# Performance work log

Measured on AMD Instinct MI355X. Metric: run time of the kernel, lower is better.

Reference implementation:

```python
import jax, jax.numpy as jnp
import numpy as np

N_NODES = 20000
OUT_DEG = 16
E = N_NODES * OUT_DEG          # 320000 directed edges
F = 20                          # edge_features
H3 = 3 * F


def _lin(key, fan_in, fan_out):
    kw, kb = jax.random.split(key)
    bound = 1.0 / np.sqrt(fan_in)
    W = jax.random.uniform(kw, (fan_in, fan_out), jnp.float32, -bound, bound)
    b = jax.random.uniform(kb, (fan_out,), jnp.float32, -bound, bound)
    return W, b


def setup_inputs() -> dict:
    key = jax.random.key(0)
    rng = np.random.default_rng(0)
    # graph: every node has exactly OUT_DEG out-edges, no self-loops
    src = np.repeat(np.arange(N_NODES, dtype=np.int64), OUT_DEG)
    dst = (src + 1 + rng.integers(0, N_NODES - 1, size=E)) % N_NODES
    edge_index = jnp.asarray(np.stack([src, dst]), dtype=jnp.int32)
    # edge adjacency per _build_edge_adj: edge i=(u->v) pairs with each out-edge j of v.
    # Edges are grouped by src, so out-edges of node v are [v*OUT_DEG, v*OUT_DEG+OUT_DEG).
    # No self-loops => i != j always, so exactly E*OUT_DEG pairs.
    adj_src = jnp.asarray(np.repeat(np.arange(E, dtype=np.int64), OUT_DEG).astype(np.int32))
    adj_nbr = jnp.asarray((dst[:, None] * OUT_DEG + np.arange(OUT_DEG)).reshape(-1).astype(np.int32))

    ks = jax.random.split(key, 8)
    edge_attr = jax.random.normal(ks[0], (E, F), jnp.float32)
    msg_W1, msg_b1 = _lin(ks[1], 2 * F, 32)
    msg_W2, msg_b2 = _lin(ks[2], 32, F)
    # torch GRUCell params: weight_ih/hh are [3H, H]
    bound = 1.0 / np.sqrt(F)
    g = jax.random.split(ks[3], 4)
    gru_Wih = jax.random.uniform(g[0], (H3, F), jnp.float32, -bound, bound)
    gru_Whh = jax.random.uniform(g[1], (H3, F), jnp.float32, -bound, bound)
    gru_bih = jax.random.uniform(g[2], (H3,), jnp.float32, -bound, bound)
    gru_bhh = jax.random.uniform(g[3], (H3,), jnp.float32, -bound, bound)
    ro_W1, ro_b1 = _lin(ks[4], F, 64)
    ro_W2, ro_b2 = _lin(ks[5], 64, 32)
    ro_W3, ro_b3 = _lin(ks[6], 32, 1)
    return {
        'edge_attr': edge_attr,
        'msg_W1': msg_W1, 'msg_b1': msg_b1, 'msg_W2': msg_W2, 'msg_b2': msg_b2,
        'gru_Wih': gru_Wih, 'gru_Whh': gru_Whh, 'gru_bih': gru_bih, 'gru_bhh': gru_bhh,
        'ro_W1': ro_W1, 'ro_b1': ro_b1, 'ro_W2': ro_W2, 'ro_b2': ro_b2,
        'ro_W3': ro_W3, 'ro_b3': ro_b3,
        'edge_index': edge_index, 'adj_src': adj_src, 'adj_nbr': adj_nbr,
    }


def reference(edge_attr, msg_W1, msg_b1, msg_W2, msg_b2,
              gru_Wih, gru_Whh, gru_bih, gru_bhh,
              ro_W1, ro_b1, ro_W2, ro_b2, ro_W3, ro_b3,
              edge_index, adj_src, adj_nbr):
    num_e = edge_attr.shape[0]

    def step(h, _):
        h_i = h[adj_src]                       # [P, F] gather
        h_j = h[adj_nbr]                       # [P, F] gather
        m = jnp.concatenate([h_i, h_j], axis=-1)  # [P, 2F]
        m = jax.nn.selu(m @ msg_W1 + msg_b1) @ msg_W2 + msg_b2  # [P, F]
        agg = jax.ops.segment_sum(m, adj_src, num_segments=num_e)  # scatter_add
        # torch.nn.GRUCell(agg, h)
        gi = agg @ gru_Wih.T + gru_bih
        gh = h @ gru_Whh.T + gru_bhh
        i_r, i_z, i_n = jnp.split(gi, 3, axis=-1)
        h_r, h_z, h_n = jnp.split(gh, 3, axis=-1)
        r = jax.nn.sigmoid(i_r + h_r)
        z = jax.nn.sigmoid(i_z + h_z)
        n = jnp.tanh(i_n + r * h_n)
        return (1.0 - z) * n + z * h, None

    h_t, _ = jax.lax.scan(step, edge_attr, None, length=4)
    h_base = h_t[:num_e]  # num_edges == E here
    x = jax.nn.selu(h_base @ ro_W1 + ro_b1)
    x = jax.nn.selu(x @ ro_W2 + ro_b2)
    w = jax.nn.softplus(x @ ro_W3 + ro_b3).squeeze(-1) + 0.1
    return jnp.clip(w, 0.1, 10.0)
```

## Files before the change

### kernel.cpp

```cpp
#include <hip/hip_runtime.h>
#include <hip/hip_fp16.h>

#define E_EDGES 320000
#define NF 20

typedef float v4 __attribute__((ext_vector_type(4)));
typedef float v2f __attribute__((ext_vector_type(2)));

#if defined(__has_builtin)
# if __has_builtin(__builtin_elementwise_fma)
#  define EWFMA(a,b,c) __builtin_elementwise_fma((a),(b),(c))
# endif
#endif
#ifndef EWFMA
# define EWFMA(a,b,c) ((a)*(b)+(c))
#endif
#if defined(__has_builtin)
# if __has_builtin(__builtin_elementwise_max)
#  define EWMAX(a,b) __builtin_elementwise_max((a),(b))
#  define EWMIN(a,b) __builtin_elementwise_min((a),(b))
# endif
#endif

#if defined(__has_builtin)
# if __has_builtin(__builtin_amdgcn_exp2f)
#  define EX2F(x) __builtin_amdgcn_exp2f(x)
# endif
#endif
#ifndef EX2F
# define EX2F(x) exp2f(x)
#endif

#define LOG2E_F 1.4426950408889634f
#define SELU_SCALE 1.0507009873554805f
#define SELU_ALPHA 1.6732632423543772f
#define SELU_KA (SELU_SCALE * SELU_ALPHA)
#define SELU_SC2 (SELU_SCALE / LOG2E_F)

__device__ __forceinline__ v4 bc4(float s) { return (v4){s, s, s, s}; }
__device__ __forceinline__ v4 v4z() { return (v4){0.f, 0.f, 0.f, 0.f}; }

__device__ __forceinline__ float selu_f(float x) {
    const float scale = SELU_SCALE;
    const float alpha = SELU_ALPHA;
    float p = fmaxf(x, 0.f);
    float m = fminf(x, 0.f);
    float e = __expf(m);
    return fmaf(scale, p, scale * alpha * (e - 1.f));
}
__device__ __forceinline__ float sigmoid_f(float x) {
    return 1.f / (1.f + __expf(-x));
}
__device__ __forceinline__ v4 selu4(v4 x) {
    const float scale = SELU_SCALE;
    const float ka = SELU_KA;
#ifdef EWMAX
    v4 p = EWMAX(x, v4z());
    v4 m = EWMIN(x, v4z());
#else
    v4 p = {fmaxf(x.x,0.f), fmaxf(x.y,0.f), fmaxf(x.z,0.f), fmaxf(x.w,0.f)};
    v4 m = {fminf(x.x,0.f), fminf(x.y,0.f), fminf(x.z,0.f), fminf(x.w,0.f)};
#endif
    v4 e = {__expf(m.x), __expf(m.y), __expf(m.z), __expf(m.w)};
    return EWFMA(bc4(scale), p, EWFMA(bc4(ka), e, bc4(-ka)));
}

__device__ __forceinline__ float hsum4(v4 x) {
    v2f lo = __builtin_shufflevector(x, x, 0, 1);
    v2f hi = __builtin_shufflevector(x, x, 2, 3);
    v2f h = lo + hi;
    return h.x + h.y;
}

__device__ __forceinline__ float dot20v(v4 a0, v4 a1, v4 a2, v4 a3, v4 a4,
                                        const v4* __restrict__ w) {
    v4 w0 = w[0], w1 = w[1], w2 = w[2], w3 = w[3], w4 = w[4];
    v4 x = a0 * w0;
    x = EWFMA(a1, w1, x); x = EWFMA(a2, w2, x);
    x = EWFMA(a3, w3, x); x = EWFMA(a4, w4, x);
    return hsum4(x);
}
__device__ __forceinline__ void dot20_dualv(const v4* __restrict__ w,
    v4 a0, v4 a1, v4 a2, v4 a3, v4 a4,
    v4 b0, v4 b1, v4 b2, v4 b3, v4 b4,
    float& r0, float& r1)
{
    v4 w0 = w[0], w1 = w[1], w2 = w[2], w3 = w[3], w4 = w[4];
    v4 xa = a0 * w0;
    xa = EWFMA(a1, w1, xa); xa = EWFMA(a2, w2, xa);
    xa = EWFMA(a3, w3, xa); xa = EWFMA(a4, w4, xa);
    v4 xb = b0 * w0;
    xb = EWFMA(b1, w1, xb); xb = EWFMA(b2, w2, xb);
    xb = EWFMA(b3, w3, xb); xb = EWFMA(b4, w4, xb);
    r0 = hsum4(xa);
    r1 = hsum4(xb);
}
__device__ __forceinline__ void h8_to_v4x2(uint4 r, v4& lo, v4& hi) {
    float2 fa = __half22float2(__builtin_bit_cast(__half2, r.x));
    float2 fb = __half22float2(__builtin_bit_cast(__half2, r.y));
    float2 fc = __half22float2(__builtin_bit_cast(__half2, r.z));
    float2 fd = __half22float2(__builtin_bit_cast(__half2, r.w));
    lo = (v4){fa.x, fa.y, fb.x, fb.y};
    hi = (v4){fc.x, fc.y, fd.x, fd.y};
}
__device__ __forceinline__ uint4 f8_to_h8(v4 lo, v4 hi) {
    uint4 r;
    r.x = __builtin_bit_cast(unsigned, __floats2half2_rn(lo.x, lo.y));
    r.y = __builtin_bit_cast(unsigned, __floats2half2_rn(lo.z, lo.w));
    r.z = __builtin_bit_cast(unsigned, __floats2half2_rn(hi.x, hi.y));
    r.w = __builtin_bit_cast(unsigned, __floats2half2_rn(hi.z, hi.w));
    return r;
}

#define FOR20(X) \
  X(0, v0.x) X(1, v0.y) X(2, v0.z) X(3, v0.w) \
  X(4, v1.x) X(5, v1.y) X(6, v1.z) X(7, v1.w) \
  X(8, v2.x) X(9, v2.y) X(10, v2.z) X(11, v2.w) \
  X(12, v3.x) X(13, v3.y) X(14, v3.z) X(15, v3.w) \
  X(16, v4v.x) X(17, v4v.y) X(18, v4v.z) X(19, v4v.w)

#define FOR20_2(X) \
  X(0, va0.x, vb0.x) X(1, va0.y, vb0.y) X(2, va0.z, vb0.z) X(3, va0.w, vb0.w) \
  X(4, va1.x, vb1.x) X(5, va1.y, vb1.y) X(6, va1.z, vb1.z) X(7, va1.w, vb1.w) \
  X(8, va2.x, vb2.x) X(9, va2.y, vb2.y) X(10, va2.z, vb2.z) X(11, va2.w, vb2.w) \
  X(12, va3.x, vb3.x) X(13, va3.y, vb3.y) X(14, va3.z, vb3.z) X(15, va3.w, vb3.w) \
  X(16, va4.x, vb4.x) X(17, va4.y, vb4.y) X(18, va4.z, vb4.z) X(19, va4.w, vb4.w)

#define FOR8S2(X) \
  X(0, sa0.x, sb0.x) X(1, sa0.y, sb0.y) X(2, sa0.z, sb0.z) X(3, sa0.w, sb0.w) \
  X(4, sa1.x, sb1.x) X(5, sa1.y, sb1.y) X(6, sa1.z, sb1.z) X(7, sa1.w, sb1.w)

__global__ void __launch_bounds__(256) kernel_B0(
    const float* __restrict__ h, const float* __restrict__ W1,
    const float* __restrict__ b1, __half* __restrict__ B)
{
    __shared__ __align__(16) float sw[640];
    __shared__ __align__(16) float sbias[32];
    for (int i = threadIdx.x; i < 640; i += 256) sw[i] = W1[640 + i] * LOG2E_F;
    if (threadIdx.x < 32) sbias[threadIdx.x] = b1[threadIdx.x] * LOG2E_F;
    __syncthreads();
    int e = blockIdx.x * 256 + threadIdx.x;
    const v4* hp = reinterpret_cast<const v4*>(h + (size_t)e * NF);
    v4 v0 = hp[0], v1 = hp[1], v2 = hp[2], v3 = hp[3], v4v = hp[4];
    const v4* bi = reinterpret_cast<const v4*>(sbias);
    v4 c0 = bi[0], c1 = bi[1], c2 = bi[2], c3 = bi[3],
       c4 = bi[4], c5 = bi[5], c6 = bi[6], c7 = bi[7];
    #define BSTEP(f, hf) { v4 t_ = bc4(hf); const v4* w_ = (const v4*)&sw[(f)*32]; \
        c0 = EWFMA(t_, w_[0], c0); c1 = EWFMA(t_, w_[1], c1); \
        c2 = EWFMA(t_, w_[2], c2); c3 = EWFMA(t_, w_[3], c3); \
        c4 = EWFMA(t_, w_[4], c4); c5 = EWFMA(t_, w_[5], c5); \
        c6 = EWFMA(t_, w_[6], c6); c7 = EWFMA(t_, w_[7], c7); }
    FOR20(BSTEP)
    #undef BSTEP
    uint4* Bp = reinterpret_cast<uint4*>(B + (size_t)e * 32);
    Bp[0] = f8_to_h8(c0, c1); Bp[1] = f8_to_h8(c2, c3);
    Bp[2] = f8_to_h8(c4, c5); Bp[3] = f8_to_h8(c6, c7);
}

template<bool WRITEB>
__global__ void __launch_bounds__(256) kernel_stepT(
    const float* __restrict__ h_in, float* __restrict__ h_out,
    const __half* __restrict__ Br, const int* __restrict__ dst,
    const float* __restrict__ W1, const float* __restrict__ b1,
    const float* __restrict__ W2, const float* __restrict__ b2,
    const float* __restrict__ Wih, const float* __restrict__ Whh,
    const float* __restrict__ bih, const float* __restrict__ bhh,
    __half* __restrict__ Bw)
{
    __shared__ __align__(16) float sW1[640];
    __shared__ __align__(16) float sW1h[640];
    __shared__ __align__(16) float sb1h[32];
    __shared__ __align__(16) float sW2[640];
    __shared__ __align__(16) float sb2v[20];
    __shared__ __align__(16) float sCorr[20];
    __shared__ __align__(16) float sWih[1200];
    __shared__ __align__(16) float sWhh[1200];
    __shared__ float sbih[60];
    __shared__ float sbhh[60];
    for (int i = threadIdx.x; i < 640; i += 256) {
        sW1[i] = W1[i] * LOG2E_F;
        sW2[i] = W2[i];
        if (WRITEB) sW1h[i] = W1[640 + i] * LOG2E_F;
    }
    for (int i = threadIdx.x; i < 1200; i += 256) { sWih[i] = Wih[i]; sWhh[i] = Whh[i]; }
    if (threadIdx.x < 20) sb2v[threadIdx.x] = b2[threadIdx.x];
    else if (threadIdx.x >= 64 && threadIdx.x < 124) sbih[threadIdx.x - 64] = bih[threadIdx.x - 64];
    else if (threadIdx.x >= 128 && threadIdx.x < 188) sbhh[threadIdx.x - 128] = bhh[threadIdx.x - 128];
    else if (WRITEB && threadIdx.x >= 192 && threadIdx.x < 224)
        sb1h[threadIdx.x - 192] = b1[threadIdx.x - 192] * LOG2E_F;
    __syncthreads();
    if (threadIdx.x < 20) {
        float s = 0.f;
        #pragma unroll
        for (int o = 0; o < 32; o++) s += sW2[o * 20 + threadIdx.x];
        sCorr[threadIdx.x] = 16.f * (sb2v[threadIdx.x] - SELU_KA * s);
    }
    __syncthreads();

    int t = blockIdx.x * 256 + threadIdx.x;
    int p = t >> 2;
    int q = t & 3;
    int ob = q * 8;
    int e0 = p * 2, e1 = p * 2 + 1;

    int2 dd = *reinterpret_cast<const int2*>(dst + e0);
    int d0 = dd.x, d1 = dd.y;

    const v4* hp0 = reinterpret_cast<const v4*>(h_in + (size_t)e0 * NF);
    const v4* hp1 = reinterpret_cast<const v4*>(h_in + (size_t)e1 * NF);
    v4 va0 = hp0[0], va1 = hp0[1], va2 = hp0[2], va3 = hp0[3], va4 = hp0[4];
    v4 vb0 = hp1[0], vb1 = hp1[1], vb2 = hp1[2], vb3 = hp1[3], vb4 = hp1[4];

    v4 aa0 = v4z(), aa1 = v4z(), ab0 = v4z(), ab1 = v4z();
    #define ASTEP2(f, h0, h1) { const v4* w_ = (const v4*)&sW1[(f)*32 + ob]; \
        v4 w0_ = w_[0], w1_ = w_[1]; \
        v4 t0_ = bc4(h0), t1_ = bc4(h1); \
        aa0 = EWFMA(t0_, w0_, aa0); aa1 = EWFMA(t0_, w1_, aa1); \
        ab0 = EWFMA(t1_, w0_, ab0); ab1 = EWFMA(t1_, w1_, ab1); }
    FOR20_2(ASTEP2)
    #undef ASTEP2

    const uint4* Bp0 = reinterpret_cast<const uint4*>(Br) + (size_t)d0 * 64 + q;
    const uint4* Bp1 = reinterpret_cast<const uint4*>(Br) + (size_t)d1 * 64 + q;
    v4 sa0 = v4z(), sa1 = v4z(), sb0 = v4z(), sb1 = v4z();
    {
        v4 kav = bc4(SELU_KA), scv = bc4(SELU_SC2), z4 = v4z();
        #define SELUACC(s_, a_, b_) { v4 x_ = (a_) + (b_); \
            v4 p_ = EWMAX(x_, z4); v4 m_ = EWMIN(x_, z4); \
            v4 e_ = {EX2F(m_.x), EX2F(m_.y), EX2F(m_.z), EX2F(m_.w)}; \
            s_ = EWFMA(kav, e_, s_); s_ = EWFMA(scv, p_, s_); }
        #pragma unroll 4
        for (int k = 0; k < 16; k++) {
            uint4 rA = Bp0[k * 4];
            uint4 rB = Bp1[k * 4];
            v4 loA, hiA, loB, hiB;
            h8_to_v4x2(rA, loA, hiA);
            h8_to_v4x2(rB, loB, hiB);
            SELUACC(sa0, aa0, loA);
            SELUACC(sa1, aa1, hiA);
            SELUACC(sb0, ab0, loB);
            SELUACC(sb1, ab1, hiB);
        }
        #undef SELUACC
    }

    v4 ga0 = v4z(), ga1 = v4z(), ga2 = v4z(), ga3 = v4z(), ga4 = v4z();
    v4 gb0 = v4z(), gb1 = v4z(), gb2 = v4z(), gb3 = v4z(), gb4 = v4z();
    #define AGGS2(j, c0_, c1_) { const v4* w_ = (const v4*)&sW2[(ob + (j)) * 20]; \
        v4 w0_ = w_[0], w1_ = w_[1], w2_ = w_[2], w3_ = w_[3], w4_ = w_[4]; \
        v4 u_ = bc4(c0_), vv_ = bc4(c1_); \
        ga0 = EWFMA(u_, w0_, ga0); ga1 = EWFMA(u_, w1_, ga1); ga2 = EWFMA(u_, w2_, ga2); \
        ga3 = EWFMA(u_, w3_, ga3); ga4 = EWFMA(u_, w4_, ga4); \
        gb0 = EWFMA(vv_, w0_, gb0); gb1 = EWFMA(vv_, w1_, gb1); gb2 = EWFMA(vv_, w2_, gb2); \
        gb3 = EWFMA(vv_, w3_, gb3); gb4 = EWFMA(vv_, w4_, gb4); }
    FOR8S2(AGGS2)
    #undef AGGS2

    #define BF1(r_, m_) { v4 t_ = { __shfl_xor(r_.x, m_), __shfl_xor(r_.y, m_), \
                                    __shfl_xor(r_.z, m_), __shfl_xor(r_.w, m_) }; \
                          r_ = r_ + t_; }
    #define BFLY(m_) BF1(ga0, m_) BF1(ga1, m_) BF1(ga2, m_) BF1(ga3, m_) BF1(ga4, m_) \
                     BF1(gb0, m_) BF1(gb1, m_) BF1(gb2, m_) BF1(gb3, m_) BF1(gb4, m_)
    BFLY(1)
    BFLY(2)
    #undef BFLY
    #undef BF1

    {
        const v4* cp = reinterpret_cast<const v4*>(sCorr);
        v4 c0 = cp[0], c1 = cp[1], c2 = cp[2], c3 = cp[3], c4 = cp[4];
        ga0 = ga0 + c0; ga1 = ga1 + c1; ga2 = ga2 + c2; ga3 = ga3 + c3; ga4 = ga4 + c4;
        gb0 = gb0 + c0; gb1 = gb1 + c1; gb2 = gb2 + c2; gb3 = gb3 + c3; gb4 = gb4 + c4;
    }

    v4 ba0, ba1, bb0, bb1;
    if (WRITEB) {
        const v4* b1p = reinterpret_cast<const v4*>(&sb1h[ob]);
        ba0 = b1p[0]; ba1 = b1p[1];
        bb0 = b1p[0]; bb1 = b1p[1];
    }

    for (int i = 0; i < 5; i++) {
        int c = q * 5 + i;
        float ir0, ir1, iz0, iz1, in0, in1, hr0, hr1, hz0, hz1, hn0, hn1;
        dot20_dualv((const v4*)&sWih[c * 20],        ga0, ga1, ga2, ga3, ga4,
                    gb0, gb1, gb2, gb3, gb4, ir0, ir1);
        dot20_dualv((const v4*)&sWih[(20 + c) * 20], ga0, ga1, ga2, ga3, ga4,
                    gb0, gb1, gb2, gb3, gb4, iz0, iz1);
        dot20_dualv((const v4*)&sWih[(40 + c) * 20], ga0, ga1, ga2, ga3, ga4,
                    gb0, gb1, gb2, gb3, gb4, in0, in1);
        dot20_dualv((const v4*)&sWhh[c * 20],        va0, va1, va2, va3, va4,
                    vb0, vb1, vb2, vb3, vb4, hr0, hr1);
        dot20_dualv((const v4*)&sWhh[(20 + c) * 20], va0, va1, va2, va3, va4,
                    vb0, vb1, vb2, vb3, vb4, hz0, hz1);
        dot20_dualv((const v4*)&sWhh[(40 + c) * 20], va0, va1, va2, va3, va4,
                    vb0, vb1, vb2, vb3, vb4, hn0, hn1);
        float bi_r = sbih[c], bi_z = sbih[20 + c], bi_n = sbih[40 + c];
        float bh_r = sbhh[c], bh_z = sbhh[20 + c], bh_n = sbhh[40 + c];
        float nh0, nh1;
        {
            float r = sigmoid_f(bi_r + ir0 + bh_r + hr0);
            float z = sigmoid_f(bi_z + iz0 + bh_z + hz0);
            float xn = bi_n + in0 + r * (bh_n + hn0);
            xn = fminf(fmaxf(xn, -20.f), 20.f);
            float tt = __expf(2.f * xn);
            float n = (tt - 1.f) / (tt + 1.f);
            float hc = h_in[(size_t)e0 * NF + c];
            nh0 = (1.f - z) * n + z * hc;
            h_out[(size_t)e0 * NF + c] = nh0;
        }
        {
            float r = sigmoid_f(bi_r + ir1 + bh_r + hr1);
            float z = sigmoid_f(bi_z + iz1 + bh_z + hz1);
            float xn = bi_n + in1 + r * (bh_n + hn1);
            xn = fminf(fmaxf(xn, -20.f), 20.f);
            float tt = __expf(2.f * xn);
            float n = (tt - 1.f) / (tt + 1.f);
            float hc = h_in[(size_t)e1 * NF + c];
            nh1 = (1.f - z) * n + z * hc;
            h_out[(size_t)e1 * NF + c] = nh1;
        }
        if (WRITEB) {
            #pragma unroll
            for (int qq = 0; qq < 4; ++qq) {
                float f0 = __shfl(nh0, qq, 4);
                float f1 = __shfl(nh1, qq, 4);
                const v4* wp = reinterpret_cast<const v4*>(&sW1h[(qq * 5 + i) * 32 + ob]);
                v4 w0 = wp[0], w1 = wp[1];
                v4 t0 = bc4(f0), t1 = bc4(f1);
                ba0 = EWFMA(t0, w0, ba0); ba1 = EWFMA(t0, w1, ba1);
                bb0 = EWFMA(t1, w0, bb0); bb1 = EWFMA(t1, w1, bb1);
            }
        }
    }
    if (WRITEB) {
        uint4* Bo = reinterpret_cast<uint4*>(Bw);
        Bo[(size_t)e0 * 4 + q] = f8_to_h8(ba0, ba1);
        Bo[(size_t)e1 * 4 + q] = f8_to_h8(bb0, bb1);
    }
}

__global__ void __launch_bounds__(256) kernel_readout(
    const float* __restrict__ h,
    const float* __restrict__ W1, const float* __restrict__ b1,
    const float* __restrict__ W2, const float* __restrict__ b2,
    const float* __restrict__ W3, const float* __restrict__ b3,
    float* __restrict__ out)
{
    __shared__ __align__(16) float sW1t[1280];
    __shared__ float sb1[64];
    __shared__ __align__(16) float sW2[2048];
    __shared__ __align__(16) float sb2v[32];
    __shared__ __align__(16) float sW3[32];
    __shared__ float sb3;
    for (int i = threadIdx.x; i < 1280; i += 256) {
        int f = i >> 6, o = i & 63;
        sW1t[o * 20 + f] = W1[i];
    }
    for (int i = threadIdx.x; i < 2048; i += 256) sW2[i] = W2[i];
    if (threadIdx.x < 64) sb1[threadIdx.x] = b1[threadIdx.x];
    else if (threadIdx.x >= 64 && threadIdx.x < 96) sb2v[threadIdx.x - 64] = b2[threadIdx.x - 64];
    else if (threadIdx.x >= 96 && threadIdx.x < 128) sW3[threadIdx.x - 96] = W3[threadIdx.x - 96];
    if (threadIdx.x == 128) sb3 = b3[0];
    __syncthreads();

    int e = blockIdx.x * 256 + threadIdx.x;
    const v4* hp = reinterpret_cast<const v4*>(h + (size_t)e * NF);
    v4 v0 = hp[0], v1 = hp[1], v2 = hp[2], v3 = hp[3], v4v = hp[4];

    const v4* b2p = reinterpret_cast<const v4*>(sb2v);
    v4 x20 = b2p[0], x21 = b2p[1], x22 = b2p[2], x23 = b2p[3],
       x24 = b2p[4], x25 = b2p[5], x26 = b2p[6], x27 = b2p[7];
    for (int o = 0; o < 64; o++) {
        float x1 = sb1[o] + dot20v(v0, v1, v2, v3, v4v, (const v4*)&sW1t[o * 20]);
        x1 = selu_f(x1);
        v4 xb = bc4(x1);
        const v4* w = (const v4*)&sW2[o * 32];
        x20 = EWFMA(xb, w[0], x20); x21 = EWFMA(xb, w[1], x21);
        x22 = EWFMA(xb, w[2], x22); x23 = EWFMA(xb, w[3], x23);
        x24 = EWFMA(xb, w[4], x24); x25 = EWFMA(xb, w[5], x25);
        x26 = EWFMA(xb, w[6], x26); x27 = EWFMA(xb, w[7], x27);
    }
    const v4* w3p = reinterpret_cast<const v4*>(sW3);
    v4 accv = selu4(x20) * w3p[0];
    accv = EWFMA(selu4(x21), w3p[1], accv);
    accv = EWFMA(selu4(x22), w3p[2], accv);
    accv = EWFMA(selu4(x23), w3p[3], accv);
    accv = EWFMA(selu4(x24), w3p[4], accv);
    accv = EWFMA(selu4(x25), w3p[5], accv);
    accv = EWFMA(selu4(x26), w3p[6], accv);
    accv = EWFMA(selu4(x27), w3p[7], accv);
    float acc = sb3 + hsum4(accv);
    float sp = fmaxf(acc, 0.f) + log1pf(__expf(-fabsf(acc)));
    float w = sp + 0.1f;
    w = fminf(fmaxf(w, 0.1f), 10.f);
    out[e] = w;
}

extern "C" void kernel_launch(void* const* d_in, const int* in_sizes, int n_in,
                              void* d_out, int out_size, void* d_ws, size_t ws_size,
                              hipStream_t stream) {
    const float* edge_attr = (const float*)d_in[0];
    const float* msg_W1   = (const float*)d_in[1];
    const float* msg_b1   = (const float*)d_in[2];
    const float* msg_W2   = (const float*)d_in[3];
    const float* msg_b2   = (const float*)d_in[4];
    const float* gru_Wih  = (const float*)d_in[5];
    const float* gru_Whh  = (const float*)d_in[6];
    const float* gru_bih  = (const float*)d_in[7];
    const float* gru_bhh  = (const float*)d_in[8];
    const float* ro_W1    = (const float*)d_in[9];
    const float* ro_b1    = (const float*)d_in[10];
    const float* ro_W2    = (const float*)d_in[11];
    const float* ro_b2    = (const float*)d_in[12];
    const float* ro_W3    = (const float*)d_in[13];
    const float* ro_b3    = (const float*)d_in[14];
    const int* edge_index = (const int*)d_in[15];
    const int* dst = edge_index + E_EDGES;

    float*  h_ws = (float*)d_ws;
    __half* BtA  = (__half*)(h_ws + (size_t)E_EDGES * NF);
    __half* BtB  = BtA + (size_t)E_EDGES * 32;

    size_t need = (size_t)E_EDGES * NF * sizeof(float)
                + 2 * (size_t)E_EDGES * 32 * sizeof(__half);
    bool fused = ws_size >= need;

    dim3 block(256);
    dim3 gridB(E_EDGES / 256);
    dim3 gridS(E_EDGES * 2 / 256);

    kernel_B0<<<gridB, block, 0, stream>>>(edge_attr, msg_W1, msg_b1, BtA);

    const float* hin = edge_attr;
    __half* Bin = BtA;
    __half* Bout = BtB;
    for (int s = 0; s < 4; s++) {
        if (!fused && s > 0)
            kernel_B0<<<gridB, block, 0, stream>>>(hin, msg_W1, msg_b1, BtA);
        if (fused && s < 3) {
            kernel_stepT<true><<<gridS, block, 0, stream>>>(hin, h_ws, Bin, dst,
                msg_W1, msg_b1, msg_W2, msg_b2, gru_Wih, gru_Whh, gru_bih, gru_bhh,
                Bout);
            __half* tmp = Bin; Bin = Bout; Bout = tmp;
        } else {
            kernel_stepT<false><<<gridS, block, 0, stream>>>(hin, h_ws, Bin, dst,
                msg_W1, msg_b1, msg_W2, msg_b2, gru_Wih, gru_Whh, gru_bih, gru_bhh,
                nullptr);
        }
        hin = h_ws;
    }
    kernel_readout<<<gridB, block, 0, stream>>>(h_ws, ro_W1, ro_b1, ro_W2, ro_b2,
                                                ro_W3, ro_b3, (float*)d_out);
}
```

Before: 554.8 us.

## Fuse final GRU step with readout MLP and use DPP lane reductions

The last message-passing step is merged with the readout MLP in one kernel. Each block keeps its updated hidden states in shared memory, reloads the readout weights into the same shared buffer, and splits the readout across two threads per edge. This removes one launch and the write and re-read of the final h through global memory. Cross-lane shuffles in the butterfly reduction and the broadcast are replaced with DPP moves, at the cost of added synchronisation and register pressure in the fused kernel.

```diff
diff --git a/kernel.cpp b/kernel.cpp
--- a/kernel.cpp
+++ b/kernel.cpp
@@ -40,6 +40,21 @@
 __device__ __forceinline__ v4 bc4(float s) { return (v4){s, s, s, s}; }
 __device__ __forceinline__ v4 v4z() { return (v4){0.f, 0.f, 0.f, 0.f}; }
 
+#define DPP_XOR1 0xB1
+#define DPP_XOR2 0x4E
+template<int CTRL>
+__device__ __forceinline__ float dppf(float x) {
+    return __builtin_bit_cast(float,
+        __builtin_amdgcn_update_dpp(0, __builtin_bit_cast(int, x), CTRL, 0xF, 0xF, true));
+}
+template<int CTRL>
+__device__ __forceinline__ v4 dpp4(v4 x) {
+    v4 r;
+    r.x = dppf<CTRL>(x.x); r.y = dppf<CTRL>(x.y);
+    r.z = dppf<CTRL>(x.z); r.w = dppf<CTRL>(x.w);
+    return r;
+}
+
 __device__ __forceinline__ float selu_f(float x) {
     const float scale = SELU_SCALE;
     const float alpha = SELU_ALPHA;
@@ -72,14 +87,6 @@
     return h.x + h.y;
 }
 
-__device__ __forceinline__ float dot20v(v4 a0, v4 a1, v4 a2, v4 a3, v4 a4,
-                                        const v4* __restrict__ w) {
-    v4 w0 = w[0], w1 = w[1], w2 = w[2], w3 = w[3], w4 = w[4];
-    v4 x = a0 * w0;
-    x = EWFMA(a1, w1, x); x = EWFMA(a2, w2, x);
-    x = EWFMA(a3, w3, x); x = EWFMA(a4, w4, x);
-    return hsum4(x);
-}
 __device__ __forceinline__ void dot20_dualv(const v4* __restrict__ w,
     v4 a0, v4 a1, v4 a2, v4 a3, v4 a4,
     v4 b0, v4 b1, v4 b2, v4 b3, v4 b4,
@@ -256,15 +263,16 @@
     FOR8S2(AGGS2)
     #undef AGGS2
 
-    #define BF1(r_, m_) { v4 t_ = { __shfl_xor(r_.x, m_), __shfl_xor(r_.y, m_), \
-                                    __shfl_xor(r_.z, m_), __shfl_xor(r_.w, m_) }; \
-                          r_ = r_ + t_; }
-    #define BFLY(m_) BF1(ga0, m_) BF1(ga1, m_) BF1(ga2, m_) BF1(ga3, m_) BF1(ga4, m_) \
-                     BF1(gb0, m_) BF1(gb1, m_) BF1(gb2, m_) BF1(gb3, m_) BF1(gb4, m_)
-    BFLY(1)
-    BFLY(2)
+    #define BFLY(CTRL) { \
+        ga0 = ga0 + dpp4<CTRL>(ga0); ga1 = ga1 + dpp4<CTRL>(ga1); \
+        ga2 = ga2 + dpp4<CTRL>(ga2); ga3 = ga3 + dpp4<CTRL>(ga3); \
+        ga4 = ga4 + dpp4<CTRL>(ga4); \
+        gb0 = gb0 + dpp4<CTRL>(gb0); gb1 = gb1 + dpp4<CTRL>(gb1); \
+        gb2 = gb2 + dpp4<CTRL>(gb2); gb3 = gb3 + dpp4<CTRL>(gb3); \
+        gb4 = gb4 + dpp4<CTRL>(gb4); }
+    BFLY(DPP_XOR1)
+    BFLY(DPP_XOR2)
     #undef BFLY
-    #undef BF1
 
     {
         const v4* cp = reinterpret_cast<const v4*>(sCorr);
@@ -321,16 +329,16 @@
             h_out[(size_t)e1 * NF + c] = nh1;
         }
         if (WRITEB) {
-            #pragma unroll
-            for (int qq = 0; qq < 4; ++qq) {
-                float f0 = __shfl(nh0, qq, 4);
-                float f1 = __shfl(nh1, qq, 4);
-                const v4* wp = reinterpret_cast<const v4*>(&sW1h[(qq * 5 + i) * 32 + ob]);
-                v4 w0 = wp[0], w1 = wp[1];
-                v4 t0 = bc4(f0), t1 = bc4(f1);
-                ba0 = EWFMA(t0, w0, ba0); ba1 = EWFMA(t0, w1, ba1);
-                bb0 = EWFMA(t1, w0, bb0); bb1 = EWFMA(t1, w1, bb1);
-            }
+            #define WB1(qq) { \
+                float f0_ = dppf<(qq)*0x55>(nh0); \
+                float f1_ = dppf<(qq)*0x55>(nh1); \
+                const v4* wp_ = reinterpret_cast<const v4*>(&sW1h[((qq)*5 + i) * 32 + ob]); \
+                v4 w0_ = wp_[0], w1_ = wp_[1]; \
+                v4 t0_ = bc4(f0_), t1_ = bc4(f1_); \
+                ba0 = EWFMA(t0_, w0_, ba0); ba1 = EWFMA(t0_, w1_, ba1); \
+                bb0 = EWFMA(t1_, w0_, bb0); bb1 = EWFMA(t1_, w1_, bb1); }
+            WB1(0) WB1(1) WB1(2) WB1(3)
+            #undef WB1
         }
     }
     if (WRITEB) {
@@ -340,61 +348,237 @@
     }
 }
 
-__global__ void __launch_bounds__(256) kernel_readout(
-    const float* __restrict__ h,
-    const float* __restrict__ W1, const float* __restrict__ b1,
-    const float* __restrict__ W2, const float* __restrict__ b2,
-    const float* __restrict__ W3, const float* __restrict__ b3,
+__global__ void __launch_bounds__(256) kernel_step_ro(
+    const float* __restrict__ h_in,
+    const __half* __restrict__ Br, const int* __restrict__ dst,
+    const float* __restrict__ W1, const float* __restrict__ W2, const float* __restrict__ b2,
+    const float* __restrict__ Wih, const float* __restrict__ Whh,
+    const float* __restrict__ bih, const float* __restrict__ bhh,
+    const float* __restrict__ roW1, const float* __restrict__ rob1,
+    const float* __restrict__ roW2, const float* __restrict__ rob2,
+    const float* __restrict__ roW3, const float* __restrict__ rob3,
     float* __restrict__ out)
 {
-    __shared__ __align__(16) float sW1t[1280];
-    __shared__ float sb1[64];
-    __shared__ __align__(16) float sW2[2048];
-    __shared__ __align__(16) float sb2v[32];
-    __shared__ __align__(16) float sW3[32];
-    __shared__ float sb3;
-    for (int i = threadIdx.x; i < 1280; i += 256) {
-        int f = i >> 6, o = i & 63;
-        sW1t[o * 20 + f] = W1[i];
-    }
-    for (int i = threadIdx.x; i < 2048; i += 256) sW2[i] = W2[i];
-    if (threadIdx.x < 64) sb1[threadIdx.x] = b1[threadIdx.x];
-    else if (threadIdx.x >= 64 && threadIdx.x < 96) sb2v[threadIdx.x - 64] = b2[threadIdx.x - 64];
-    else if (threadIdx.x >= 96 && threadIdx.x < 128) sW3[threadIdx.x - 96] = W3[threadIdx.x - 96];
-    if (threadIdx.x == 128) sb3 = b3[0];
+    __shared__ __align__(16) float S[3840];
+    __shared__ __align__(16) float sh[2560];
+    float* sW1  = S;
+    float* sW2  = S + 640;
+    float* sb2v = S + 1280;
+    float* sCorr= S + 1300;
+    float* sWih = S + 1320;
+    float* sWhh = S + 2520;
+    float* sbih = S + 3720;
+    float* sbhh = S + 3780;
+
+    for (int i = threadIdx.x; i < 640; i += 256) {
+        sW1[i] = W1[i] * LOG2E_F;
+        sW2[i] = W2[i];
+    }
+    for (int i = threadIdx.x; i < 1200; i += 256) { sWih[i] = Wih[i]; sWhh[i] = Whh[i]; }
+    if (threadIdx.x < 20) sb2v[threadIdx.x] = b2[threadIdx.x];
+    else if (threadIdx.x >= 64 && threadIdx.x < 124) sbih[threadIdx.x - 64] = bih[threadIdx.x - 64];
+    else if (threadIdx.x >= 128 && threadIdx.x < 188) sbhh[threadIdx.x - 128] = bhh[threadIdx.x - 128];
     __syncthreads();
-
-    int e = blockIdx.x * 256 + threadIdx.x;
-    const v4* hp = reinterpret_cast<const v4*>(h + (size_t)e * NF);
-    v4 v0 = hp[0], v1 = hp[1], v2 = hp[2], v3 = hp[3], v4v = hp[4];
-
-    const v4* b2p = reinterpret_cast<const v4*>(sb2v);
-    v4 x20 = b2p[0], x21 = b2p[1], x22 = b2p[2], x23 = b2p[3],
-       x24 = b2p[4], x25 = b2p[5], x26 = b2p[6], x27 = b2p[7];
-    for (int o = 0; o < 64; o++) {
-        float x1 = sb1[o] + dot20v(v0, v1, v2, v3, v4v, (const v4*)&sW1t[o * 20]);
-        x1 = selu_f(x1);
-        v4 xb = bc4(x1);
-        const v4* w = (const v4*)&sW2[o * 32];
-        x20 = EWFMA(xb, w[0], x20); x21 = EWFMA(xb, w[1], x21);
-        x22 = EWFMA(xb, w[2], x22); x23 = EWFMA(xb, w[3], x23);
-        x24 = EWFMA(xb, w[4], x24); x25 = EWFMA(xb, w[5], x25);
-        x26 = EWFMA(xb, w[6], x26); x27 = EWFMA(xb, w[7], x27);
-    }
-    const v4* w3p = reinterpret_cast<const v4*>(sW3);
-    v4 accv = selu4(x20) * w3p[0];
-    accv = EWFMA(selu4(x21), w3p[1], accv);
-    accv = EWFMA(selu4(x22), w3p[2], accv);
-    accv = EWFMA(selu4(x23), w3p[3], accv);
-    accv = EWFMA(selu4(x24), w3p[4], accv);
-    accv = EWFMA(selu4(x25), w3p[5], accv);
-    accv = EWFMA(selu4(x26), w3p[6], accv);
-    accv = EWFMA(selu4(x27), w3p[7], accv);
-    float acc = sb3 + hsum4(accv);
-    float sp = fmaxf(acc, 0.f) + log1pf(__expf(-fabsf(acc)));
-    float w = sp + 0.1f;
-    w = fminf(fmaxf(w, 0.1f), 10.f);
-    out[e] = w;
+    if (threadIdx.x < 20) {
+        float s = 0.f;
+        #pragma unroll
+        for (int o = 0; o < 32; o++) s += sW2[o * 20 + threadIdx.x];
+        sCorr[threadIdx.x] = 16.f * (sb2v[threadIdx.x] - SELU_KA * s);
+    }
+    __syncthreads();
+
+    int t = blockIdx.x * 256 + threadIdx.x;
+    int p = t >> 2;
+    int q = t & 3;
+    int ob = q * 8;
+    int e0 = p * 2, e1 = p * 2 + 1;
+    int lp = threadIdx.x >> 2;
+    int el0 = lp * 2, el1 = lp * 2 + 1;
+
+    int2 dd = *reinterpret_cast<const int2*>(dst + e0);
+    int d0 = dd.x, d1 = dd.y;
+
+    const v4* hp0 = reinterpret_cast<const v4*>(h_in + (size_t)e0 * NF);
+    const v4* hp1 = reinterpret_cast<const v4*>(h_in + (size_t)e1 * NF);
+    v4 va0 = hp0[0], va1 = hp0[1], va2 = hp0[2], va3 = hp0[3], va4 = hp0[4];
+    v4 vb0 = hp1[0], vb1 = hp1[1], vb2 = hp1[2], vb3 = hp1[3], vb4 = hp1[4];
+
+    v4 aa0 = v4z(), aa1 = v4z(), ab0 = v4z(), ab1 = v4z();
+    #define ASTEP2(f, h0, h1) { const v4* w_ = (const v4*)&sW1[(f)*32 + ob]; \
+        v4 w0_ = w_[0], w1_ = w_[1]; \
+        v4 t0_ = bc4(h0), t1_ = bc4(h1); \
+        aa0 = EWFMA(t0_, w0_, aa0); aa1 = EWFMA(t0_, w1_, aa1); \
+        ab0 = EWFMA(t1_, w0_, ab0); ab1 = EWFMA(t1_, w1_, ab1); }
+    FOR20_2(ASTEP2)
+    #undef ASTEP2
+
+    const uint4* Bp0 = reinterpret_cast<const uint4*>(Br) + (size_t)d0 * 64 + q;
+    const uint4* Bp1 = reinterpret_cast<const uint4*>(Br) + (size_t)d1 * 64 + q;
+    v4 sa0 = v4z(), sa1 = v4z(), sb0 = v4z(), sb1 = v4z();
+    {
+        v4 kav = bc4(SELU_KA), scv = bc4(SELU_SC2), z4 = v4z();
+        #define SELUACC(s_, a_, b_) { v4 x_ = (a_) + (b_); \
+            v4 p_ = EWMAX(x_, z4); v4 m_ = EWMIN(x_, z4); \
+            v4 e_ = {EX2F(m_.x), EX2F(m_.y), EX2F(m_.z), EX2F(m_.w)}; \
+            s_ = EWFMA(kav, e_, s_); s_ = EWFMA(scv, p_, s_); }
+        #pragma unroll 4
+        for (int k = 0; k < 16; k++) {
+            uint4 rA = Bp0[k * 4];
+            uint4 rB = Bp1[k * 4];
+            v4 loA, hiA, loB, hiB;
+            h8_to_v4x2(rA, loA, hiA);
+            h8_to_v4x2(rB, loB, hiB);
+            SELUACC(sa0, aa0, loA);
+            SELUACC(sa1, aa1, hiA);
+            SELUACC(sb0, ab0, loB);
+            SELUACC(sb1, ab1, hiB);
+        }
+        #undef SELUACC
+    }
+
+    v4 ga0 = v4z(), ga1 = v4z(), ga2 = v4z(), ga3 = v4z(), ga4 = v4z();
+    v4 gb0 = v4z(), gb1 = v4z(), gb2 = v4z(), gb3 = v4z(), gb4 = v4z();
+    #define AGGS2(j, c0_, c1_) { const v4* w_ = (const v4*)&sW2[(ob + (j)) * 20]; \
+        v4 w0_ = w_[0], w1_ = w_[1], w2_ = w_[2], w3_ = w_[3], w4_ = w_[4]; \
+        v4 u_ = bc4(c0_), vv_ = bc4(c1_); \
+        ga0 = EWFMA(u_, w0_, ga0); ga1 = EWFMA(u_, w1_, ga1); ga2 = EWFMA(u_, w2_, ga2); \
+        ga3 = EWFMA(u_, w3_, ga3); ga4 = EWFMA(u_, w4_, ga4); \
+        gb0 = EWFMA(vv_, w0_, gb0); gb1 = EWFMA(vv_, w1_, gb1); gb2 = EWFMA(vv_, w2_, gb2); \
+        gb3 = EWFMA(vv_, w3_, gb3); gb4 = EWFMA(vv_, w4_, gb4); }
+    FOR8S2(AGGS2)
+    #undef AGGS2
+
+    #define BFLY(CTRL) { \
+        ga0 = ga0 + dpp4<CTRL>(ga0); ga1 = ga1 + dpp4<CTRL>(ga1); \
+        ga2 = ga2 + dpp4<CTRL>(ga2); ga3 = ga3 + dpp4<CTRL>(ga3); \
+        ga4 = ga4 + dpp4<CTRL>(ga4); \
+        gb0 = gb0 + dpp4<CTRL>(gb0); gb1 = gb1 + dpp4<CTRL>(gb1); \
+        gb2 = gb2 + dpp4<CTRL>(gb2); gb3 = gb3 + dpp4<CTRL>(gb3); \
+        gb4 = gb4 + dpp4<CTRL>(gb4); }
+    BFLY(DPP_XOR1)
+    BFLY(DPP_XOR2)
+    #undef BFLY
+
+    {
+        const v4* cp = reinterpret_cast<const v4*>(sCorr);
+        v4 c0 = cp[0], c1 = cp[1], c2 = cp[2], c3 = cp[3], c4 = cp[4];
+        ga0 = ga0 + c0; ga1 = ga1 + c1; ga2 = ga2 + c2; ga3 = ga3 + c3; ga4 = ga4 + c4;
+        gb0 = gb0 + c0; gb1 = gb1 + c1; gb2 = gb2 + c2; gb3 = gb3 + c3; gb4 = gb4 + c4;
+    }
+
+    for (int i = 0; i < 5; i++) {
+        int c = q * 5 + i;
+        float ir0, ir1, iz0, iz1, in0, in1, hr0, hr1, hz0, hz1, hn0, hn1;
+        dot20_dualv((const v4*)&sWih[c * 20],        ga0, ga1, ga2, ga3, ga4,
+                    gb0, gb1, gb2, gb3, gb4, ir0, ir1);
+        dot20_dualv((const v4*)&sWih[(20 + c) * 20], ga0, ga1, ga2, ga3, ga4,
+                    gb0, gb1, gb2, gb3, gb4, iz0, iz1);
+        dot20_dualv((const v4*)&sWih[(40 + c) * 20], ga0, ga1, ga2, ga3, ga4,
+                    gb0, gb1, gb2, gb3, gb4, in0, in1);
+        dot20_dualv((const v4*)&sWhh[c * 20],        va0, va1, va2, va3, va4,
+                    vb0, vb1, vb2, vb3, vb4, hr0, hr1);
+        dot20_dualv((const v4*)&sWhh[(20 + c) * 20], va0, va1, va2, va3, va4,
+                    vb0, vb1, vb2, vb3, vb4, hz0, hz1);
+        dot20_dualv((const v4*)&sWhh[(40 + c) * 20], va0, va1, va2, va3, va4,
+                    vb0, vb1, vb2, vb3, vb4, hn0, hn1);
+        float bi_r = sbih[c], bi_z = sbih[20 + c], bi_n = sbih[40 + c];
+        float bh_r = sbhh[c], bh_z = sbhh[20 + c], bh_n = sbhh[40 + c];
+        {
+            float r = sigmoid_f(bi_r + ir0 + bh_r + hr0);
+            float z = sigmoid_f(bi_z + iz0 + bh_z + hz0);
+            float xn = bi_n + in0 + r * (bh_n + hn0);
+            xn = fminf(fmaxf(xn, -20.f), 20.f);
+            float tt = __expf(2.f * xn);
+            float n = (tt - 1.f) / (tt + 1.f);
+            float hc = h_in[(size_t)e0 * NF + c];
+            sh[el0 * 20 + c] = (1.f - z) * n + z * hc;
+        }
+        {
+            float r = sigmoid_f(bi_r + ir1 + bh_r + hr1);
+            float z = sigmoid_f(bi_z + iz1 + bh_z + hz1);
+            float xn = bi_n + in1 + r * (bh_n + hn1);
+            xn = fminf(fmaxf(xn, -20.f), 20.f);
+            float tt = __expf(2.f * xn);
+            float n = (tt - 1.f) / (tt + 1.f);
+            float hc = h_in[(size_t)e1 * NF + c];
+            sh[el1 * 20 + c] = (1.f - z) * n + z * hc;
+        }
+    }
+
+    __syncthreads();
+    for (int i = threadIdx.x; i < 1280; i += 256) S[i] = roW1[i];
+    for (int i = threadIdx.x; i < 2048; i += 256) S[1344 + i] = roW2[i];
+    {
+        int tx = threadIdx.x;
+        if (tx < 64) S[1280 + tx] = rob1[tx];
+        else if (tx < 96) S[3392 + (tx - 64)] = rob2[tx - 64];
+        else if (tx < 128) S[3424 + (tx - 96)] = roW3[tx - 96];
+        else if (tx == 128) S[3456] = rob3[0];
+    }
+    __syncthreads();
+
+    {
+        int el = threadIdx.x >> 1;
+        int half = threadIdx.x & 1;
+        int ob32 = half * 32;
+        const v4* hp = reinterpret_cast<const v4*>(&sh[el * 20]);
+        v4 v0 = hp[0], v1 = hp[1], v2 = hp[2], v3 = hp[3], v4v = hp[4];
+
+        const v4* b1p = reinterpret_cast<const v4*>(&S[1280 + ob32]);
+        v4 x0 = b1p[0], x1 = b1p[1], x2 = b1p[2], x3 = b1p[3],
+           x4 = b1p[4], x5 = b1p[5], x6 = b1p[6], x7 = b1p[7];
+        #define ROS(f, hf) { v4 t_ = bc4(hf); const v4* w_ = (const v4*)&S[(f)*64 + ob32]; \
+            x0 = EWFMA(t_, w_[0], x0); x1 = EWFMA(t_, w_[1], x1); \
+            x2 = EWFMA(t_, w_[2], x2); x3 = EWFMA(t_, w_[3], x3); \
+            x4 = EWFMA(t_, w_[4], x4); x5 = EWFMA(t_, w_[5], x5); \
+            x6 = EWFMA(t_, w_[6], x6); x7 = EWFMA(t_, w_[7], x7); }
+        FOR20(ROS)
+        #undef ROS
+        x0 = selu4(x0); x1 = selu4(x1); x2 = selu4(x2); x3 = selu4(x3);
+        x4 = selu4(x4); x5 = selu4(x5); x6 = selu4(x6); x7 = selu4(x7);
+
+        const v4* b2p = reinterpret_cast<const v4*>(&S[3392]);
+        v4 y0, y1, y2, y3, y4, y5, y6, y7;
+        if (half == 0) {
+            y0 = b2p[0]; y1 = b2p[1]; y2 = b2p[2]; y3 = b2p[3];
+            y4 = b2p[4]; y5 = b2p[5]; y6 = b2p[6]; y7 = b2p[7];
+        } else {
+            y0 = v4z(); y1 = v4z(); y2 = v4z(); y3 = v4z();
+            y4 = v4z(); y5 = v4z(); y6 = v4z(); y7 = v4z();
+        }
+        #define Y8(s_, o_) { const v4* w_ = reinterpret_cast<const v4*>(&S[1344 + (o_)*32]); \
+            v4 t_ = bc4(s_); \
+            y0 = EWFMA(t_, w_[0], y0); y1 = EWFMA(t_, w_[1], y1); \
+            y2 = EWFMA(t_, w_[2], y2); y3 = EWFMA(t_, w_[3], y3); \
+            y4 = EWFMA(t_, w_[4], y4); y5 = EWFMA(t_, w_[5], y5); \
+            y6 = EWFMA(t_, w_[6], y6); y7 = EWFMA(t_, w_[7], y7); }
+        #define S2V(jj, xv) Y8(xv.x, ob32+(jj)*4+0) Y8(xv.y, ob32+(jj)*4+1) \
+                            Y8(xv.z, ob32+(jj)*4+2) Y8(xv.w, ob32+(jj)*4+3)
+        S2V(0, x0) S2V(1, x1) S2V(2, x2) S2V(3, x3)
+        S2V(4, x4) S2V(5, x5) S2V(6, x6) S2V(7, x7)
+        #undef S2V
+        #undef Y8
+
+        y0 = y0 + dpp4<DPP_XOR1>(y0); y1 = y1 + dpp4<DPP_XOR1>(y1);
+        y2 = y2 + dpp4<DPP_XOR1>(y2); y3 = y3 + dpp4<DPP_XOR1>(y3);
+        y4 = y4 + dpp4<DPP_XOR1>(y4); y5 = y5 + dpp4<DPP_XOR1>(y5);
+        y6 = y6 + dpp4<DPP_XOR1>(y6); y7 = y7 + dpp4<DPP_XOR1>(y7);
+
+        const v4* w3p = reinterpret_cast<const v4*>(&S[3424]);
+        v4 accv = selu4(y0) * w3p[0];
+        accv = EWFMA(selu4(y1), w3p[1], accv);
+        accv = EWFMA(selu4(y2), w3p[2], accv);
+        accv = EWFMA(selu4(y3), w3p[3], accv);
+        accv = EWFMA(selu4(y4), w3p[4], accv);
+        accv = EWFMA(selu4(y5), w3p[5], accv);
+        accv = EWFMA(selu4(y6), w3p[6], accv);
+        accv = EWFMA(selu4(y7), w3p[7], accv);
+        float acc = S[3456] + hsum4(accv);
+        float sp = fmaxf(acc, 0.f) + log1pf(__expf(-fabsf(acc)));
+        float wv = sp + 0.1f;
+        wv = fminf(fmaxf(wv, 0.1f), 10.f);
+        if (half == 0) out[blockIdx.x * 128 + el] = wv;
+    }
 }
 
 extern "C" void kernel_launch(void* const* d_in, const int* in_sizes, int n_in,
@@ -435,10 +619,10 @@
     const float* hin = edge_attr;
     __half* Bin = BtA;
     __half* Bout = BtB;
-    for (int s = 0; s < 4; s++) {
+    for (int s = 0; s < 3; s++) {
         if (!fused && s > 0)
             kernel_B0<<<gridB, block, 0, stream>>>(hin, msg_W1, msg_b1, BtA);
-        if (fused && s < 3) {
+        if (fused) {
             kernel_stepT<true><<<gridS, block, 0, stream>>>(hin, h_ws, Bin, dst,
                 msg_W1, msg_b1, msg_W2, msg_b2, gru_Wih, gru_Whh, gru_bih, gru_bhh,
                 Bout);
@@ -450,6 +634,9 @@
         }
         hin = h_ws;
     }
-    kernel_readout<<<gridB, block, 0, stream>>>(h_ws, ro_W1, ro_b1, ro_W2, ro_b2,
-                                                ro_W3, ro_b3, (float*)d_out);
-}
+    if (!fused)
+        kernel_B0<<<gridB, block, 0, stream>>>(hin, msg_W1, msg_b1, BtA);
+    kernel_step_ro<<<gridS, block, 0, stream>>>(hin, Bin, dst,
+        msg_W1, msg_W2, msg_b2, gru_Wih, gru_Whh, gru_bih, gru_bhh,
+        ro_W1, ro_b1, ro_W2, ro_b2, ro_W3, ro_b3, (float*)d_out);
+}
```

Result: slower. 848.1 us (+52.9%).
